# Kernel tuning notes

Hardware: AMD Instinct MI355X
Metric: run time of the kernel (lower is better)

The kernel has to match this reference:

```python
import jax, jax.numpy as jnp
import numpy as np

ALPHA = 0.2  # LeakyReLU negative slope


def setup_inputs() -> dict:
    key = jax.random.key(0)
    ks = jax.random.split(key, 8)
    B, S, T, V, F = 8, 25, 64, 256, 256
    N = S * T
    h = jax.random.normal(ks[0], (B, S, T, V), dtype=jnp.float32)
    adj = jax.random.randint(ks[1], (N, N), 0, 2, dtype=jnp.int32)
    # xavier-ish scaling for stability
    W = jax.random.normal(ks[2], (F, V), dtype=jnp.float32) * (1.414 / np.sqrt(V))
    bW = jax.random.normal(ks[3], (F,), dtype=jnp.float32) * 0.01
    ai = jax.random.normal(ks[4], (1, F), dtype=jnp.float32) * (1.414 / np.sqrt(F))
    bi = jax.random.normal(ks[5], (1,), dtype=jnp.float32) * 0.01
    aj = jax.random.normal(ks[6], (1, F), dtype=jnp.float32) * (1.414 / np.sqrt(F))
    bj = jax.random.normal(ks[7], (1,), dtype=jnp.float32) * 0.01
    return {"h": h, "adj": adj, "W": W, "bW": bW, "ai": ai, "bi": bi, "aj": aj, "bj": bj}


def reference(h, adj, W, bW, ai, bi, aj, bj):
    B, S, T, V = h.shape
    N = S * T
    x = h.reshape(B, N, V)                    # [B, N, V]
    Wh = jnp.einsum('bnv,fv->bnf', x, W) + bW  # [B, N, F]
    Wh1 = jnp.einsum('bnf,of->bno', Wh, ai) + bi  # [B, N, 1]
    Wh2 = jnp.einsum('bnf,of->bno', Wh, aj) + bj  # [B, N, 1]
    e = Wh1 + jnp.swapaxes(Wh2, 1, 2)          # [B, N, N] additive scores
    e = jnp.where(e > 0, e, ALPHA * e)         # LeakyReLU
    att = jnp.where(adj[None, :, :] > 0, e, jnp.float32(-1e9))
    att = jax.nn.softmax(att, axis=2)          # masked softmax over neighbors
    h_hat = jnp.einsum('bij,bjf->bif', att, Wh)  # [B, N, F]
    return jax.nn.elu(h_hat)                   # concat=True path
```

## Files before the change

### kernel.cpp

```cpp
#include <hip/hip_runtime.h>
#include <hip/hip_bf16.h>

typedef __attribute__((ext_vector_type(8))) short bf16x8;
typedef __attribute__((ext_vector_type(4))) float f32x4;

#define LRELU_ALPHA 0.2f

__device__ __forceinline__ unsigned short f2bf(float x) {
    unsigned u = __float_as_uint(x);
    u += 0x7fffu + ((u >> 16) & 1u);
    return (unsigned short)(u >> 16);
}

__global__ __launch_bounds__(256) void k_gemm_wh(
    const float* __restrict__ x, const float* __restrict__ W,
    const float* __restrict__ bW, float* __restrict__ Wh)
{
    __shared__ alignas(16) float As[32][132];
    __shared__ alignas(16) float Bs[32][132];
    const int t  = threadIdx.x;
    const int r0 = blockIdx.x * 128;
    const int f0 = blockIdx.y * 128;
    const int tx = t & 15, ty = t >> 4;
    const int li = t >> 3;
    const int lk = (t & 7) << 2;

    float acc[8][8];
#pragma unroll
    for (int i = 0; i < 8; ++i)
#pragma unroll
        for (int j = 0; j < 8; ++j) acc[i][j] = 0.f;

    for (int k0 = 0; k0 < 256; k0 += 32) {
        float4 av[4], bv[4];
#pragma unroll
        for (int q = 0; q < 4; ++q) {
            av[q] = *(const float4*)&x[(size_t)(r0 + li + 32*q)*256 + k0 + lk];
            bv[q] = *(const float4*)&W[(size_t)(f0 + li + 32*q)*256 + k0 + lk];
        }
        __syncthreads();
#pragma unroll
        for (int q = 0; q < 4; ++q) {
            const float* a = (const float*)&av[q];
            const float* b = (const float*)&bv[q];
#pragma unroll
            for (int e = 0; e < 4; ++e) {
                As[lk + e][li + 32*q] = a[e];
                Bs[lk + e][li + 32*q] = b[e];
            }
        }
        __syncthreads();
#pragma unroll
        for (int kk = 0; kk < 32; ++kk) {
            float a[8], b[8];
            *(float4*)&a[0] = *(const float4*)&As[kk][4*tx ? 4*ty : 4*ty];
            *(float4*)&a[0] = *(const float4*)&As[kk][4*ty];
            *(float4*)&a[4] = *(const float4*)&As[kk][64 + 4*ty];
            *(float4*)&b[0] = *(const float4*)&Bs[kk][4*tx];
            *(float4*)&b[4] = *(const float4*)&Bs[kk][64 + 4*tx];
#pragma unroll
            for (int i = 0; i < 8; ++i)
#pragma unroll
                for (int j = 0; j < 8; ++j)
                    acc[i][j] = __builtin_fmaf(a[i], b[j], acc[i][j]);
        }
    }
    float4 bw0 = *(const float4*)&bW[f0 + 4*tx];
    float4 bw1 = *(const float4*)&bW[f0 + 64 + 4*tx];
#pragma unroll
    for (int ah = 0; ah < 2; ++ah)
#pragma unroll
        for (int e = 0; e < 4; ++e) {
            int r = r0 + ah*64 + 4*ty + e;
            float4 v0, v1;
            v0.x = acc[ah*4+e][0] + bw0.x; v0.y = acc[ah*4+e][1] + bw0.y;
            v0.z = acc[ah*4+e][2] + bw0.z; v0.w = acc[ah*4+e][3] + bw0.w;
            v1.x = acc[ah*4+e][4] + bw1.x; v1.y = acc[ah*4+e][5] + bw1.y;
            v1.z = acc[ah*4+e][6] + bw1.z; v1.w = acc[ah*4+e][7] + bw1.w;
            *(float4*)&Wh[(size_t)r*256 + f0 + 4*tx] = v0;
            *(float4*)&Wh[(size_t)r*256 + f0 + 64 + 4*tx] = v1;
        }
}

__global__ __launch_bounds__(256) void k_rowdots(
    const float* __restrict__ Wh, const float* __restrict__ ai,
    const float* __restrict__ bi, const float* __restrict__ aj,
    const float* __restrict__ bj,
    float* __restrict__ Wh1, float* __restrict__ Wh2)
{
    const int lane = threadIdx.x & 63;
    const int r = blockIdx.x * 4 + (threadIdx.x >> 6);
    float4 w4 = *(const float4*)&Wh[(size_t)r*256 + lane*4];
    float4 a4 = *(const float4*)&ai[lane*4];
    float4 c4 = *(const float4*)&aj[lane*4];
    float s1 = w4.x*a4.x + w4.y*a4.y + w4.z*a4.z + w4.w*a4.w;
    float s2 = w4.x*c4.x + w4.y*c4.y + w4.z*c4.z + w4.w*c4.w;
#pragma unroll
    for (int m = 1; m < 64; m <<= 1) {
        s1 += __shfl_xor(s1, m, 64);
        s2 += __shfl_xor(s2, m, 64);
    }
    if (lane == 0) {
        Wh1[r] = s1 + bi[0];
        Wh2[r] = s2 + bj[0];
    }
}

__global__ __launch_bounds__(256) void k_transpose(
    const float* __restrict__ Wh, unsigned short* __restrict__ WhT)
{
    __shared__ alignas(16) unsigned short tile[64][72];
    const int t = threadIdx.x;
    const int n0 = blockIdx.x * 64, f0 = blockIdx.y * 64, b = blockIdx.z;
    const int fi = (t & 15) * 4;
    const int i0 = t >> 4;
#pragma unroll
    for (int q = 0; q < 4; ++q) {
        int i = i0 + 16*q;
        float4 v = *(const float4*)&Wh[(size_t)(b*1600 + n0 + i)*256 + f0 + fi];
        tile[fi+0][i] = f2bf(v.x);
        tile[fi+1][i] = f2bf(v.y);
        tile[fi+2][i] = f2bf(v.z);
        tile[fi+3][i] = f2bf(v.w);
    }
    __syncthreads();
    const int f = t >> 2;
    const int nq = t & 3;
    int4 u0 = *(const int4*)&tile[f][nq*16];
    int4 u1 = *(const int4*)&tile[f][nq*16 + 8];
    size_t o = (size_t)(b*256 + f0 + f)*1600 + n0 + nq*16;
    *(int4*)&WhT[o] = u0;
    *(int4*)&WhT[o + 8] = u1;
}

__global__ __launch_bounds__(256) void k_attn(
    const unsigned short* __restrict__ WhT,
    const float* __restrict__ Wh1, const float* __restrict__ Wh2,
    const int* __restrict__ adj, float* __restrict__ out)
{
    __shared__ alignas(16) unsigned short whs[256*64];
    __shared__ alignas(16) unsigned short pls[32*64];
    __shared__ float scale_s[32];
    __shared__ float l_s[32];

    const int t = threadIdx.x;
    const int w = t >> 6;
    const int l = t & 63;
    const int b = blockIdx.y;
    const int i0 = blockIdx.x * 32;

    const int jj16 = l & 15;
    const int rr = (l >> 4) & 3;
    const int row0 = w*8 + rr*2;
    float wh1v[2];
    wh1v[0] = Wh1[b*1600 + i0 + row0 + 0];
    wh1v[1] = Wh1[b*1600 + i0 + row0 + 1];
    float m_r[2] = {-INFINITY, -INFINITY};
    float l_r[2] = {0.f, 0.f};

    const int cl = l & 15;
    const int kg = l >> 4;
    f32x4 acc[2][4];
#pragma unroll
    for (int a = 0; a < 2; ++a)
#pragma unroll
        for (int c = 0; c < 4; ++c) acc[a][c] = (f32x4){0.f, 0.f, 0.f, 0.f};

    const unsigned short* whtb = WhT + (size_t)b * 256 * 1600;
    const int sfr = w*8 + (l >> 3);
    const int sc_ = l & 7;

    for (int jt = 0; jt < 25; ++jt) {
        const int j0 = jt * 64;
#pragma unroll
        for (int q = 0; q < 8; ++q) {
            int f = q*32 + sfr;
            int cs = sc_ ^ (f & 7);
            const unsigned short* g = whtb + (size_t)f*1600 + j0 + cs*8;
            unsigned short* lp = &whs[(q*32 + w*8) * 64];
            __builtin_amdgcn_global_load_lds(
                (const __attribute__((address_space(1))) unsigned int*)g,
                (__attribute__((address_space(3))) unsigned int*)lp, 16, 0, 0);
        }
        float4 wh2 = *(const float4*)&Wh2[b*1600 + j0 + jj16*4];
        const float* w2 = (const float*)&wh2;
#pragma unroll
        for (int r = 0; r < 2; ++r) {
            const int gi = i0 + row0 + r;
            int4 a4 = *(const int4*)&adj[(size_t)gi*1600 + j0 + jj16*4];
            const int* am = (const int*)&a4;
            float s[4];
#pragma unroll
            for (int q = 0; q < 4; ++q) {
                float raw = wh1v[r] + w2[q];
                float lr = raw > 0.f ? raw : LRELU_ALPHA * raw;
                s[q] = (am[q] > 0) ? lr : -1e9f;
            }
            float tmax = fmaxf(fmaxf(s[0], s[1]), fmaxf(s[2], s[3]));
#pragma unroll
            for (int m = 1; m < 16; m <<= 1)
                tmax = fmaxf(tmax, __shfl_xor(tmax, m, 64));
            float mnew = fmaxf(m_r[r], tmax);
            float fac = __expf(m_r[r] - mnew);
            float p0 = __expf(s[0]-mnew), p1 = __expf(s[1]-mnew);
            float p2 = __expf(s[2]-mnew), p3 = __expf(s[3]-mnew);
            float tsum = (p0+p1)+(p2+p3);
#pragma unroll
            for (int m = 1; m < 16; m <<= 1)
                tsum += __shfl_xor(tsum, m, 64);
            l_r[r] = l_r[r]*fac + tsum;
            m_r[r] = mnew;
            const int i = row0 + r;
            ushort4 pk;
            pk.x = f2bf(p0); pk.y = f2bf(p1); pk.z = f2bf(p2); pk.w = f2bf(p3);
            int off = i*128 + jj16*8;
            off ^= (i & 7) << 4;
            *(ushort4*)((char*)pls + off) = pk;
            if (jj16 == 0) {
                scale_s[i] = fac;
                if (jt == 24) l_s[i] = l_r[r];
            }
        }
        asm volatile("s_waitcnt vmcnt(0)" ::: "memory");
        __syncthreads();
#pragma unroll
        for (int mi = 0; mi < 2; ++mi)
#pragma unroll
            for (int rg = 0; rg < 4; ++rg) {
                float sc = scale_s[mi*16 + kg*4 + rg];
#pragma unroll
                for (int nf = 0; nf < 4; ++nf) acc[mi][nf][rg] *= sc;
            }
#pragma unroll
        for (int kb = 0; kb < 2; ++kb) {
            bf16x8 af[2], bfr[4];
#pragma unroll
            for (int mi = 0; mi < 2; ++mi) {
                int i = mi*16 + cl;
                int off = i*128 + kb*64 + kg*16;
                off ^= (i & 7) << 4;
                af[mi] = *(const bf16x8*)((const char*)pls + off);
            }
#pragma unroll
            for (int nf = 0; nf < 4; ++nf) {
                int f = w*64 + nf*16 + cl;
                int off = f*128 + kb*64 + kg*16;
                off ^= (f & 7) << 4;
                bfr[nf] = *(const bf16x8*)((const char*)whs + off);
            }
#pragma unroll
            for (int mi = 0; mi < 2; ++mi)
#pragma unroll
                for (int nf = 0; nf < 4; ++nf)
                    acc[mi][nf] = __builtin_amdgcn_mfma_f32_16x16x32_bf16(
                        af[mi], bfr[nf], acc[mi][nf], 0, 0, 0);
        }
        __syncthreads();
    }
#pragma unroll
    for (int mi = 0; mi < 2; ++mi)
#pragma unroll
        for (int rg = 0; rg < 4; ++rg) {
            int i = mi*16 + kg*4 + rg;
            float rl = 1.f / l_s[i];
#pragma unroll
            for (int nf = 0; nf < 4; ++nf) {
                float v = acc[mi][nf][rg] * rl;
                v = v > 0.f ? v : expm1f(v);
                out[(size_t)(b*1600 + i0 + i)*256 + w*64 + nf*16 + cl] = v;
            }
        }
}

extern "C" void kernel_launch(void* const* d_in, const int* in_sizes, int n_in,
                              void* d_out, int out_size, void* d_ws, size_t ws_size,
                              hipStream_t stream)
{
    const float* h  = (const float*)d_in[0];
    const int* adj  = (const int*)d_in[1];
    const float* W  = (const float*)d_in[2];
    const float* bW = (const float*)d_in[3];
    const float* ai = (const float*)d_in[4];
    const float* bi = (const float*)d_in[5];
    const float* aj = (const float*)d_in[6];
    const float* bj = (const float*)d_in[7];
    float* out = (float*)d_out;

    char* ws = (char*)d_ws;
    float* Wh = (float*)ws;
    unsigned short* WhT = (unsigned short*)(ws + 13107200);
    float* Wh1 = (float*)(ws + 13107200 + 6553600);
    float* Wh2 = Wh1 + 12800;

    k_gemm_wh<<<dim3(100, 2), 256, 0, stream>>>(h, W, bW, Wh);
    k_rowdots<<<3200, 256, 0, stream>>>(Wh, ai, bi, aj, bj, Wh1, Wh2);
    k_transpose<<<dim3(25, 4, 8), 256, 0, stream>>>(Wh, WhT);
    k_attn<<<dim3(50, 8), 256, 0, stream>>>(WhT, Wh1, Wh2, adj, out);
}
```

Measured before the change: 178.7 us.

## Fuse projection GEMM with rowdots and transpose; precompute exact row max for softmax

New measurement: 214.6 us. 20.1% more time.

```diff
diff --git a/kernel.cpp b/kernel.cpp
--- a/kernel.cpp
+++ b/kernel.cpp
@@ -12,263 +12,215 @@
     return (unsigned short)(u >> 16);
 }
 
-__global__ __launch_bounds__(256) void k_gemm_wh(
+__global__ __launch_bounds__(256) void k_gemm_fused(
     const float* __restrict__ x, const float* __restrict__ W,
-    const float* __restrict__ bW, float* __restrict__ Wh)
-{
-    __shared__ alignas(16) float As[32][132];
-    __shared__ alignas(16) float Bs[32][132];
-    const int t  = threadIdx.x;
-    const int r0 = blockIdx.x * 128;
-    const int f0 = blockIdx.y * 128;
-    const int tx = t & 15, ty = t >> 4;
-    const int li = t >> 3;
-    const int lk = (t & 7) << 2;
-
-    float acc[8][8];
-#pragma unroll
-    for (int i = 0; i < 8; ++i)
-#pragma unroll
-        for (int j = 0; j < 8; ++j) acc[i][j] = 0.f;
-
-    for (int k0 = 0; k0 < 256; k0 += 32) {
-        float4 av[4], bv[4];
-#pragma unroll
-        for (int q = 0; q < 4; ++q) {
-            av[q] = *(const float4*)&x[(size_t)(r0 + li + 32*q)*256 + k0 + lk];
-            bv[q] = *(const float4*)&W[(size_t)(f0 + li + 32*q)*256 + k0 + lk];
-        }
-        __syncthreads();
-#pragma unroll
-        for (int q = 0; q < 4; ++q) {
-            const float* a = (const float*)&av[q];
-            const float* b = (const float*)&bv[q];
-#pragma unroll
-            for (int e = 0; e < 4; ++e) {
-                As[lk + e][li + 32*q] = a[e];
-                Bs[lk + e][li + 32*q] = b[e];
-            }
-        }
-        __syncthreads();
-#pragma unroll
-        for (int kk = 0; kk < 32; ++kk) {
-            float a[8], b[8];
-            *(float4*)&a[0] = *(const float4*)&As[kk][4*tx ? 4*ty : 4*ty];
-            *(float4*)&a[0] = *(const float4*)&As[kk][4*ty];
-            *(float4*)&a[4] = *(const float4*)&As[kk][64 + 4*ty];
-            *(float4*)&b[0] = *(const float4*)&Bs[kk][4*tx];
-            *(float4*)&b[4] = *(const float4*)&Bs[kk][64 + 4*tx];
-#pragma unroll
-            for (int i = 0; i < 8; ++i)
-#pragma unroll
-                for (int j = 0; j < 8; ++j)
-                    acc[i][j] = __builtin_fmaf(a[i], b[j], acc[i][j]);
-        }
-    }
-    float4 bw0 = *(const float4*)&bW[f0 + 4*tx];
-    float4 bw1 = *(const float4*)&bW[f0 + 64 + 4*tx];
-#pragma unroll
-    for (int ah = 0; ah < 2; ++ah)
-#pragma unroll
-        for (int e = 0; e < 4; ++e) {
-            int r = r0 + ah*64 + 4*ty + e;
-            float4 v0, v1;
-            v0.x = acc[ah*4+e][0] + bw0.x; v0.y = acc[ah*4+e][1] + bw0.y;
-            v0.z = acc[ah*4+e][2] + bw0.z; v0.w = acc[ah*4+e][3] + bw0.w;
-            v1.x = acc[ah*4+e][4] + bw1.x; v1.y = acc[ah*4+e][5] + bw1.y;
-            v1.z = acc[ah*4+e][6] + bw1.z; v1.w = acc[ah*4+e][7] + bw1.w;
-            *(float4*)&Wh[(size_t)r*256 + f0 + 4*tx] = v0;
-            *(float4*)&Wh[(size_t)r*256 + f0 + 64 + 4*tx] = v1;
-        }
-}
-
-__global__ __launch_bounds__(256) void k_rowdots(
-    const float* __restrict__ Wh, const float* __restrict__ ai,
+    const float* __restrict__ bW, const float* __restrict__ ai,
     const float* __restrict__ bi, const float* __restrict__ aj,
     const float* __restrict__ bj,
-    float* __restrict__ Wh1, float* __restrict__ Wh2)
-{
-    const int lane = threadIdx.x & 63;
-    const int r = blockIdx.x * 4 + (threadIdx.x >> 6);
-    float4 w4 = *(const float4*)&Wh[(size_t)r*256 + lane*4];
-    float4 a4 = *(const float4*)&ai[lane*4];
-    float4 c4 = *(const float4*)&aj[lane*4];
-    float s1 = w4.x*a4.x + w4.y*a4.y + w4.z*a4.z + w4.w*a4.w;
-    float s2 = w4.x*c4.x + w4.y*c4.y + w4.z*c4.z + w4.w*c4.w;
-#pragma unroll
-    for (int m = 1; m < 64; m <<= 1) {
-        s1 += __shfl_xor(s1, m, 64);
-        s2 += __shfl_xor(s2, m, 64);
-    }
-    if (lane == 0) {
-        Wh1[r] = s1 + bi[0];
-        Wh2[r] = s2 + bj[0];
-    }
-}
-
-__global__ __launch_bounds__(256) void k_transpose(
-    const float* __restrict__ Wh, unsigned short* __restrict__ WhT)
-{
-    __shared__ alignas(16) unsigned short tile[64][72];
+    unsigned short* __restrict__ WhT, float* __restrict__ Wh1,
+    float* __restrict__ Wh2)
+{
+    __shared__ alignas(16) unsigned short As[32*40];
+    __shared__ alignas(16) unsigned short Bs[256*40];
+    __shared__ float part1[2][32], part2[2][32];
+
     const int t = threadIdx.x;
-    const int n0 = blockIdx.x * 64, f0 = blockIdx.y * 64, b = blockIdx.z;
-    const int fi = (t & 15) * 4;
-    const int i0 = t >> 4;
-#pragma unroll
-    for (int q = 0; q < 4; ++q) {
-        int i = i0 + 16*q;
-        float4 v = *(const float4*)&Wh[(size_t)(b*1600 + n0 + i)*256 + f0 + fi];
-        tile[fi+0][i] = f2bf(v.x);
-        tile[fi+1][i] = f2bf(v.y);
-        tile[fi+2][i] = f2bf(v.z);
-        tile[fi+3][i] = f2bf(v.w);
-    }
+    const int w = t >> 6, l = t & 63;
+    const int wr = w >> 1, wc = w & 1;
+    const int R0 = blockIdx.x * 32;
+
+    const int srow = t >> 3;
+    const int sk4  = (t & 7) * 4;
+
+    f32x4 acc[8];
+#pragma unroll
+    for (int nf = 0; nf < 8; ++nf) acc[nf] = (f32x4){0.f,0.f,0.f,0.f};
+
+    for (int k0 = 0; k0 < 256; k0 += 32) {
+        float4 av = *(const float4*)&x[(size_t)(R0 + srow)*256 + k0 + sk4];
+        float4 bv[8];
+#pragma unroll
+        for (int q = 0; q < 8; ++q)
+            bv[q] = *(const float4*)&W[(size_t)(q*32 + srow)*256 + k0 + sk4];
+        __syncthreads();
+        ushort4 a4 = { f2bf(av.x), f2bf(av.y), f2bf(av.z), f2bf(av.w) };
+        *(ushort4*)&As[srow*40 + sk4] = a4;
+#pragma unroll
+        for (int q = 0; q < 8; ++q) {
+            ushort4 b4 = { f2bf(bv[q].x), f2bf(bv[q].y), f2bf(bv[q].z), f2bf(bv[q].w) };
+            *(ushort4*)&Bs[(q*32 + srow)*40 + sk4] = b4;
+        }
+        __syncthreads();
+        bf16x8 af = *(const bf16x8*)&As[(wr*16 + (l&15))*40 + (l>>4)*8];
+#pragma unroll
+        for (int nf = 0; nf < 8; ++nf) {
+            bf16x8 bfv = *(const bf16x8*)&Bs[(wc*128 + nf*16 + (l&15))*40 + (l>>4)*8];
+            acc[nf] = __builtin_amdgcn_mfma_f32_16x16x32_bf16(af, bfv, acc[nf], 0, 0, 0);
+        }
+    }
+
+    const int b   = R0 / 1600;
+    const int n0b = R0 - b*1600;
+    const int rowg = wr*16 + (l>>4)*4;
+    float p1[4] = {0,0,0,0}, p2[4] = {0,0,0,0};
+#pragma unroll
+    for (int nf = 0; nf < 8; ++nf) {
+        const int f = wc*128 + nf*16 + (l & 15);
+        const float bwv = bW[f], aiv = ai[f], ajv = aj[f];
+        float vv[4];
+#pragma unroll
+        for (int e = 0; e < 4; ++e) {
+            float v = acc[nf][e] + bwv;
+            vv[e] = v;
+            p1[e] = __builtin_fmaf(v, aiv, p1[e]);
+            p2[e] = __builtin_fmaf(v, ajv, p2[e]);
+        }
+        ushort4 o4 = { f2bf(vv[0]), f2bf(vv[1]), f2bf(vv[2]), f2bf(vv[3]) };
+        *(ushort4*)&WhT[((size_t)(b*256 + f))*1600 + n0b + rowg] = o4;
+    }
+#pragma unroll
+    for (int m = 1; m < 16; m <<= 1)
+#pragma unroll
+        for (int e = 0; e < 4; ++e) {
+            p1[e] += __shfl_xor(p1[e], m, 64);
+            p2[e] += __shfl_xor(p2[e], m, 64);
+        }
+    if ((l & 15) == 0)
+#pragma unroll
+        for (int e = 0; e < 4; ++e) {
+            part1[wc][rowg + e] = p1[e];
+            part2[wc][rowg + e] = p2[e];
+        }
     __syncthreads();
-    const int f = t >> 2;
-    const int nq = t & 3;
-    int4 u0 = *(const int4*)&tile[f][nq*16];
-    int4 u1 = *(const int4*)&tile[f][nq*16 + 8];
-    size_t o = (size_t)(b*256 + f0 + f)*1600 + n0 + nq*16;
-    *(int4*)&WhT[o] = u0;
-    *(int4*)&WhT[o + 8] = u1;
-}
-
-__global__ __launch_bounds__(256) void k_attn(
+    if (t < 32) {
+        Wh1[R0 + t] = part1[0][t] + part1[1][t] + bi[0];
+        Wh2[R0 + t] = part2[0][t] + part2[1][t] + bj[0];
+    }
+}
+
+__global__ __launch_bounds__(256) void k_m2(
+    const int* __restrict__ adj, const float* __restrict__ Wh2,
+    float* __restrict__ M2)
+{
+    const int w = threadIdx.x >> 6, l = threadIdx.x & 63;
+    const int i = blockIdx.x * 4 + w;
+    float m[8];
+#pragma unroll
+    for (int b = 0; b < 8; ++b) m[b] = -3.0e38f;
+    for (int j0 = 0; j0 < 1600; j0 += 64) {
+        int a = adj[(size_t)i*1600 + j0 + l];
+#pragma unroll
+        for (int b = 0; b < 8; ++b) {
+            float v = Wh2[b*1600 + j0 + l];
+            m[b] = (a > 0) ? fmaxf(m[b], v) : m[b];
+        }
+    }
+#pragma unroll
+    for (int s = 1; s < 64; s <<= 1)
+#pragma unroll
+        for (int b = 0; b < 8; ++b)
+            m[b] = fmaxf(m[b], __shfl_xor(m[b], s, 64));
+    if (l == 0)
+#pragma unroll
+        for (int b = 0; b < 8; ++b)
+            M2[b*1600 + i] = m[b];
+}
+
+__global__ __launch_bounds__(512) void k_attn(
     const unsigned short* __restrict__ WhT,
-    const float* __restrict__ Wh1, const float* __restrict__ Wh2,
-    const int* __restrict__ adj, float* __restrict__ out)
+    const float* __restrict__ Wh1, const float* __restrict__ M2,
+    const float* __restrict__ Wh2, const int* __restrict__ adj,
+    float* __restrict__ out)
 {
     __shared__ alignas(16) unsigned short whs[256*64];
     __shared__ alignas(16) unsigned short pls[32*64];
-    __shared__ float scale_s[32];
     __shared__ float l_s[32];
 
     const int t = threadIdx.x;
-    const int w = t >> 6;
-    const int l = t & 63;
-    const int b = blockIdx.y;
-    const int i0 = blockIdx.x * 32;
-
-    const int jj16 = l & 15;
-    const int rr = (l >> 4) & 3;
-    const int row0 = w*8 + rr*2;
-    float wh1v[2];
-    wh1v[0] = Wh1[b*1600 + i0 + row0 + 0];
-    wh1v[1] = Wh1[b*1600 + i0 + row0 + 1];
-    float m_r[2] = {-INFINITY, -INFINITY};
-    float l_r[2] = {0.f, 0.f};
-
-    const int cl = l & 15;
-    const int kg = l >> 4;
-    f32x4 acc[2][4];
-#pragma unroll
-    for (int a = 0; a < 2; ++a)
-#pragma unroll
-        for (int c = 0; c < 4; ++c) acc[a][c] = (f32x4){0.f, 0.f, 0.f, 0.f};
-
-    const unsigned short* whtb = WhT + (size_t)b * 256 * 1600;
-    const int sfr = w*8 + (l >> 3);
+    const int w = t >> 6, l = t & 63;
+    const int bid = blockIdx.x;
+    const int b = bid & 7;
+    const int i0 = (bid >> 3) * 32;
+    const int wr = w >> 2, wc = w & 3;
+
+    float wh1r[4], mr[4];
+#pragma unroll
+    for (int r = 0; r < 4; ++r) {
+        int gi = i0 + w*4 + r;
+        wh1r[r] = Wh1[b*1600 + gi];
+        float s = wh1r[r] + M2[b*1600 + gi];
+        mr[r] = s > 0.f ? s : LRELU_ALPHA * s;
+    }
+    float lsum[4] = {0,0,0,0};
+    f32x4 acc[4];
+#pragma unroll
+    for (int nf = 0; nf < 4; ++nf) acc[nf] = (f32x4){0.f,0.f,0.f,0.f};
+
+    const unsigned short* whtb = WhT + (size_t)b*256*1600;
+    const int sfr = w*8 + (l>>3);
     const int sc_ = l & 7;
 
     for (int jt = 0; jt < 25; ++jt) {
         const int j0 = jt * 64;
 #pragma unroll
-        for (int q = 0; q < 8; ++q) {
-            int f = q*32 + sfr;
+        for (int q = 0; q < 4; ++q) {
+            int f = q*64 + sfr;
             int cs = sc_ ^ (f & 7);
             const unsigned short* g = whtb + (size_t)f*1600 + j0 + cs*8;
-            unsigned short* lp = &whs[(q*32 + w*8) * 64];
+            unsigned short* lp = &whs[(q*64 + w*8)*64];
             __builtin_amdgcn_global_load_lds(
                 (const __attribute__((address_space(1))) unsigned int*)g,
                 (__attribute__((address_space(3))) unsigned int*)lp, 16, 0, 0);
         }
-        float4 wh2 = *(const float4*)&Wh2[b*1600 + j0 + jj16*4];
-        const float* w2 = (const float*)&wh2;
-#pragma unroll
-        for (int r = 0; r < 2; ++r) {
-            const int gi = i0 + row0 + r;
-            int4 a4 = *(const int4*)&adj[(size_t)gi*1600 + j0 + jj16*4];
-            const int* am = (const int*)&a4;
-            float s[4];
-#pragma unroll
-            for (int q = 0; q < 4; ++q) {
-                float raw = wh1v[r] + w2[q];
-                float lr = raw > 0.f ? raw : LRELU_ALPHA * raw;
-                s[q] = (am[q] > 0) ? lr : -1e9f;
+        float wh2l = Wh2[b*1600 + j0 + l];
+#pragma unroll
+        for (int r = 0; r < 4; ++r) {
+            const int row = w*4 + r;
+            int a = adj[(size_t)(i0 + row)*1600 + j0 + l];
+            float s = wh1r[r] + wh2l;
+            s = s > 0.f ? s : LRELU_ALPHA * s;
+            float p = (a > 0) ? __expf(s - mr[r]) : 0.f;
+            lsum[r] += p;
+            int off = (row*128 + l*2) ^ ((row & 7) << 4);
+            *(unsigned short*)((char*)pls + off) = f2bf(p);
+        }
+        asm volatile("s_waitcnt vmcnt(0)" ::: "memory");
+        __syncthreads();
+#pragma unroll
+        for (int kb = 0; kb < 2; ++kb) {
+            const int arow = wr*16 + (l & 15);
+            int aoff = (arow*128 + kb*64 + (l>>4)*16) ^ ((arow & 7) << 4);
+            bf16x8 af = *(const bf16x8*)((const char*)pls + aoff);
+#pragma unroll
+            for (int nf = 0; nf < 4; ++nf) {
+                int f = wc*64 + nf*16 + (l & 15);
+                int boff = (f*128 + kb*64 + (l>>4)*16) ^ ((f & 7) << 4);
+                bf16x8 bfv = *(const bf16x8*)((const char*)whs + boff);
+                acc[nf] = __builtin_amdgcn_mfma_f32_16x16x32_bf16(af, bfv, acc[nf], 0, 0, 0);
             }
-            float tmax = fmaxf(fmaxf(s[0], s[1]), fmaxf(s[2], s[3]));
-#pragma unroll
-            for (int m = 1; m < 16; m <<= 1)
-                tmax = fmaxf(tmax, __shfl_xor(tmax, m, 64));
-            float mnew = fmaxf(m_r[r], tmax);
-            float fac = __expf(m_r[r] - mnew);
-            float p0 = __expf(s[0]-mnew), p1 = __expf(s[1]-mnew);
-            float p2 = __expf(s[2]-mnew), p3 = __expf(s[3]-mnew);
-            float tsum = (p0+p1)+(p2+p3);
-#pragma unroll
-            for (int m = 1; m < 16; m <<= 1)
-                tsum += __shfl_xor(tsum, m, 64);
-            l_r[r] = l_r[r]*fac + tsum;
-            m_r[r] = mnew;
-            const int i = row0 + r;
-            ushort4 pk;
-            pk.x = f2bf(p0); pk.y = f2bf(p1); pk.z = f2bf(p2); pk.w = f2bf(p3);
-            int off = i*128 + jj16*8;
-            off ^= (i & 7) << 4;
-            *(ushort4*)((char*)pls + off) = pk;
-            if (jj16 == 0) {
-                scale_s[i] = fac;
-                if (jt == 24) l_s[i] = l_r[r];
-            }
-        }
-        asm volatile("s_waitcnt vmcnt(0)" ::: "memory");
-        __syncthreads();
-#pragma unroll
-        for (int mi = 0; mi < 2; ++mi)
-#pragma unroll
-            for (int rg = 0; rg < 4; ++rg) {
-                float sc = scale_s[mi*16 + kg*4 + rg];
-#pragma unroll
-                for (int nf = 0; nf < 4; ++nf) acc[mi][nf][rg] *= sc;
-            }
-#pragma unroll
-        for (int kb = 0; kb < 2; ++kb) {
-            bf16x8 af[2], bfr[4];
-#pragma unroll
-            for (int mi = 0; mi < 2; ++mi) {
-                int i = mi*16 + cl;
-                int off = i*128 + kb*64 + kg*16;
-                off ^= (i & 7) << 4;
-                af[mi] = *(const bf16x8*)((const char*)pls + off);
-            }
-#pragma unroll
-            for (int nf = 0; nf < 4; ++nf) {
-                int f = w*64 + nf*16 + cl;
-                int off = f*128 + kb*64 + kg*16;
-                off ^= (f & 7) << 4;
-                bfr[nf] = *(const bf16x8*)((const char*)whs + off);
-            }
-#pragma unroll
-            for (int mi = 0; mi < 2; ++mi)
-#pragma unroll
-                for (int nf = 0; nf < 4; ++nf)
-                    acc[mi][nf] = __builtin_amdgcn_mfma_f32_16x16x32_bf16(
-                        af[mi], bfr[nf], acc[mi][nf], 0, 0, 0);
-        }
-        __syncthreads();
-    }
-#pragma unroll
-    for (int mi = 0; mi < 2; ++mi)
-#pragma unroll
-        for (int rg = 0; rg < 4; ++rg) {
-            int i = mi*16 + kg*4 + rg;
-            float rl = 1.f / l_s[i];
-#pragma unroll
-            for (int nf = 0; nf < 4; ++nf) {
-                float v = acc[mi][nf][rg] * rl;
-                v = v > 0.f ? v : expm1f(v);
-                out[(size_t)(b*1600 + i0 + i)*256 + w*64 + nf*16 + cl] = v;
-            }
+        }
+        __syncthreads();
+    }
+#pragma unroll
+    for (int s = 1; s < 64; s <<= 1)
+#pragma unroll
+        for (int r = 0; r < 4; ++r)
+            lsum[r] += __shfl_xor(lsum[r], s, 64);
+    if (l == 0)
+#pragma unroll
+        for (int r = 0; r < 4; ++r) l_s[w*4 + r] = lsum[r];
+    __syncthreads();
+    float rl[4];
+#pragma unroll
+    for (int e = 0; e < 4; ++e) rl[e] = 1.f / l_s[wr*16 + (l>>4)*4 + e];
+#pragma unroll
+    for (int nf = 0; nf < 4; ++nf)
+#pragma unroll
+        for (int e = 0; e < 4; ++e) {
+            int row = wr*16 + (l>>4)*4 + e;
+            float v = acc[nf][e] * rl[e];
+            v = v > 0.f ? v : expm1f(v);
+            out[(size_t)(b*1600 + i0 + row)*256 + wc*64 + nf*16 + (l & 15)] = v;
         }
 }
 
@@ -287,13 +239,12 @@
     float* out = (float*)d_out;
 
     char* ws = (char*)d_ws;
-    float* Wh = (float*)ws;
-    unsigned short* WhT = (unsigned short*)(ws + 13107200);
-    float* Wh1 = (float*)(ws + 13107200 + 6553600);
+    unsigned short* WhT = (unsigned short*)ws;
+    float* Wh1 = (float*)(ws + 6553600);
     float* Wh2 = Wh1 + 12800;
-
-    k_gemm_wh<<<dim3(100, 2), 256, 0, stream>>>(h, W, bW, Wh);
-    k_rowdots<<<3200, 256, 0, stream>>>(Wh, ai, bi, aj, bj, Wh1, Wh2);
-    k_transpose<<<dim3(25, 4, 8), 256, 0, stream>>>(Wh, WhT);
-    k_attn<<<dim3(50, 8), 256, 0, stream>>>(WhT, Wh1, Wh2, adj, out);
-}
+    float* M2  = Wh2 + 12800;
+
+    k_gemm_fused<<<400, 256, 0, stream>>>(h, W, bW, ai, bi, aj, bj, WhT, Wh1, Wh2);
+    k_m2<<<400, 256, 0, stream>>>(adj, Wh2, M2);
+    k_attn<<<400, 512, 0, stream>>>(WhT, Wh1, M2, Wh2, adj, out);
+}
```
